# Performance work log

Hardware: AMD Instinct MI355X
Metric: run time of the kernel (lower is better)

## Reference

```python
import jax, jax.numpy as jnp
import numpy as np

N_NODES = 100000
N_EDGES = 800000
N_LABEL = 262144
IN, H, OUT = 16, 256, 128
BN_EPS = 1e-5


def setup_inputs() -> dict:
    key = jax.random.key(0)
    ks = jax.random.split(key, 32)
    def lin(k, fi, fo):
        return jax.random.normal(k, (fi, fo), jnp.float32) / np.sqrt(fi)
    inp = {
        "x": jax.random.normal(ks[0], (N_NODES, IN), jnp.float32),
        "edge_index": jax.random.randint(ks[1], (2, N_EDGES), 0, N_NODES, jnp.int32),
        "edge_weight": jax.random.uniform(ks[2], (N_EDGES,), jnp.float32),
        "edge_label_index": jax.random.randint(ks[3], (2, N_LABEL), 0, N_NODES, jnp.int32),
        # encoder GCN layers: 4 convs, BN on first 3
        "W1": lin(ks[4], IN, H),  "b1": jnp.zeros((H,), jnp.float32),
        "g1": jnp.ones((H,), jnp.float32), "be1": jnp.zeros((H,), jnp.float32),
        "W2": lin(ks[5], H, H),   "b2": jnp.zeros((H,), jnp.float32),
        "g2": jnp.ones((H,), jnp.float32), "be2": jnp.zeros((H,), jnp.float32),
        "W3": lin(ks[6], H, H),   "b3": jnp.zeros((H,), jnp.float32),
        "g3": jnp.ones((H,), jnp.float32), "be3": jnp.zeros((H,), jnp.float32),
        "W4": lin(ks[7], H, OUT), "b4": jnp.zeros((OUT,), jnp.float32),
        # decoder MLP on concatenated pair embeddings
        "D1W": lin(ks[8], 2 * OUT, OUT), "D1b": jnp.zeros((OUT,), jnp.float32),
        "D2W": lin(ks[9], OUT, OUT),     "D2b": jnp.zeros((OUT,), jnp.float32),
        "D3W": lin(ks[10], OUT, 1),      "D3b": jnp.zeros((1,), jnp.float32),
    }
    return inp


def _forward(x, edge_index, edge_weight, edge_label_index,
             W1, b1, g1, be1, W2, b2, g2, be2, W3, b3, g3, be3, W4, b4,
             D1W, D1b, D2W, D2b, D3W, D3b):
    n = x.shape[0]
    src, dst = edge_index[0], edge_index[1]
    # GCN symmetric normalization with self-loops (weight 1)
    deg = jax.ops.segment_sum(edge_weight, dst, num_segments=n) + 1.0
    dinv = jax.lax.rsqrt(deg)
    edge_norm = dinv[src] * edge_weight * dinv[dst]   # [E]
    self_norm = dinv * dinv                            # [N]

    def gcn(h, W, b):
        h = h @ W                                      # [N, F]
        agg = jax.ops.segment_sum(h[src] * edge_norm[:, None], dst, num_segments=n)
        return agg + h * self_norm[:, None] + b

    def bn(h, g, be):  # training-mode BatchNorm1d over node dim
        m = h.mean(axis=0)
        v = h.var(axis=0)
        return (h - m) * jax.lax.rsqrt(v + BN_EPS) * g + be

    h = jax.nn.relu(bn(gcn(x, W1, b1), g1, be1))
    h = jax.nn.relu(bn(gcn(h, W2, b2), g2, be2))
    h = jax.nn.relu(bn(gcn(h, W3, b3), g3, be3))
    z = gcn(h, W4, b4)                                 # [N, OUT] encoded

    # decode: gather both endpoints, concat, MLP + sigmoid
    e0, e1 = edge_label_index[0], edge_label_index[1]
    q = jnp.concatenate([z[e0], z[e1]], axis=1)        # [EL, 2*OUT]
    q = jax.nn.relu(q @ D1W + D1b)
    q = jax.nn.relu(q @ D2W + D2b)
    p = jax.nn.sigmoid(q @ D3W + D3b)
    return p.squeeze(-1)                               # [EL]


def reference(x, edge_index, edge_weight, edge_label_index,
              W1, b1, g1, be1, W2, b2, g2, be2, W3, b3, g3, be3, W4, b4,
              D1W, D1b, D2W, D2b, D3W, D3b):
    return _forward(x, edge_index, edge_weight, edge_label_index,
                    W1, b1, g1, be1, W2, b2, g2, be2, W3, b3, g3, be3, W4, b4,
                    D1W, D1b, D2W, D2b, D3W, D3b)
```

## Files before the change

kernel.cpp:

```cpp
#include <hip/hip_runtime.h>
#include <cmath>

#define NN 100000
#define NE 800000
#define NL 262144
#define GB 782
#define NP1 3125

typedef __attribute__((ext_vector_type(8))) short bf16x8;
typedef __attribute__((ext_vector_type(4))) float f32x4;

__device__ __forceinline__ unsigned short f2bf(float f) {
  unsigned int u = __builtin_bit_cast(unsigned int, f);
  u = (u + 0x7FFF + ((u >> 16) & 1)) >> 16;
  return (unsigned short)u;
}
__device__ __forceinline__ float bf2f(unsigned short u) {
  return __builtin_bit_cast(float, (unsigned int)u << 16);
}

__global__ void k_degcnt(const int* __restrict__ dst, const float* __restrict__ w,
                         unsigned long long* __restrict__ dc) {
  int e = blockIdx.x * 256 + threadIdx.x;
  if (e < NE) {
    unsigned long long pk = (1ULL << 32) | (unsigned long long)(unsigned int)(w[e] * 8388608.0f);
    atomicAdd(&dc[dst[e]], pk);
  }
}
__global__ void k_dinv2(const unsigned long long* __restrict__ dc,
                        float* __restrict__ dinv, int* __restrict__ cnt) {
  int n = blockIdx.x * 256 + threadIdx.x;
  if (n < NN) {
    unsigned long long v = dc[n];
    cnt[n] = (int)(v >> 32);
    dinv[n] = rsqrtf((float)(unsigned int)v * (1.0f / 8388608.0f) + 1.0f);
  }
}
__global__ void k_scan1(const int* __restrict__ cnt, int* __restrict__ tsum) {
  __shared__ int s[256];
  int t = threadIdx.x;
  int base = blockIdx.x * 1024;
  int acc = 0;
  for (int i = 0; i < 4; i++) { int idx = base + t * 4 + i; if (idx < NN) acc += cnt[idx]; }
  s[t] = acc; __syncthreads();
  for (int o = 128; o > 0; o >>= 1) { if (t < o) s[t] += s[t + o]; __syncthreads(); }
  if (t == 0) tsum[blockIdx.x] = s[0];
}
__global__ void k_scan2(const int* __restrict__ tsum, int* __restrict__ toff, int nt, int* __restrict__ rowptr_end) {
  __shared__ int s[256];
  int t = threadIdx.x;
  int v = (t < nt) ? tsum[t] : 0;
  s[t] = v; __syncthreads();
  for (int o = 1; o < 256; o <<= 1) { int xv = (t >= o) ? s[t - o] : 0; __syncthreads(); s[t] += xv; __syncthreads(); }
  if (t < nt) toff[t] = s[t] - v;
  if (t == 255) *rowptr_end = s[255];
}
__global__ void k_scan3(const int* __restrict__ cnt, const int* __restrict__ toff,
                        int* __restrict__ rowptr, int* __restrict__ nxt) {
  __shared__ int s[256];
  int t = threadIdx.x;
  int base = blockIdx.x * 1024 + t * 4;
  int v[4]; int tot = 0;
  for (int i = 0; i < 4; i++) { int idx = base + i; v[i] = (idx < NN) ? cnt[idx] : 0; tot += v[i]; }
  s[t] = tot; __syncthreads();
  for (int o = 1; o < 256; o <<= 1) { int xv = (t >= o) ? s[t - o] : 0; __syncthreads(); s[t] += xv; __syncthreads(); }
  int excl = s[t] - tot + toff[blockIdx.x];
  for (int i = 0; i < 4; i++) {
    int idx = base + i;
    if (idx < NN) { rowptr[idx] = excl; nxt[idx] = excl; }
    excl += v[i];
  }
}
__global__ void k_scatter2(const int* __restrict__ src, const int* __restrict__ dst, const float* __restrict__ w,
                           const float* __restrict__ dinv, int* __restrict__ nxt,
                           int* __restrict__ esp, float* __restrict__ enp) {
  int e = blockIdx.x * 256 + threadIdx.x;
  if (e < NE) {
    int d = dst[e], s = src[e];
    int p = atomicAdd(&nxt[d], 1);
    esp[p] = s; enp[p] = dinv[s] * w[e] * dinv[d];
  }
}

__global__ void k_cvt_wT(const float* __restrict__ W, unsigned short* __restrict__ Wt, int K, int N) {
  int id = blockIdx.x * 256 + threadIdx.x;
  if (id >= K * N) return;
  int n = id / K, k = id - n * K;
  Wt[id] = f2bf(W[k * N + n]);
}
__global__ void k_cvt_d1(const float* __restrict__ D1W, unsigned short* __restrict__ Wt) {
  int id = blockIdx.x * 256 + threadIdx.x;
  if (id >= 256 * 128) return;
  int n = id >> 7, k = id & 127;
  float v = (n < 128) ? D1W[(size_t)k * 128 + n] : D1W[(size_t)(128 + k) * 128 + (n - 128)];
  Wt[id] = f2bf(v);
}
__global__ void k_biasuv(const float* __restrict__ D1b, float* __restrict__ buv) {
  int t = threadIdx.x;
  buv[t] = (t < 128) ? D1b[t] : 0.f;
}

__global__ void k_pack(const unsigned short* __restrict__ Wt, unsigned short* __restrict__ P, int K, int NJ) {
  int id = blockIdx.x * 256 + threadIdx.x;
  int total = (K / 32) * NJ * 64;
  if (id >= total) return;
  int lane = id & 63, g = id >> 6;
  int j = g % NJ, s = g / NJ;
  int fr = lane & 15, fq = lane >> 4;
  uint4 v = *(const uint4*)(Wt + (size_t)(j * 16 + fr) * K + s * 32 + fq * 8);
  *(uint4*)(P + (size_t)id * 8) = v;
}

__global__ __launch_bounds__(256) void k_agg16(const float* __restrict__ x,
    const int* __restrict__ esp, const float* __restrict__ enp,
    const int* __restrict__ rowptr, const float* __restrict__ dinv,
    float* __restrict__ ax) {
  const int t = threadIdx.x;
  const int lane = t & 63;
  const int g = lane >> 2, gl = lane & 3;
  const int n = blockIdx.x * 64 + (t >> 6) * 16 + g;
  if (n >= NN) return;
  const float4* x4 = (const float4*)x;
  float d = dinv[n]; float dd = d * d;
  float4 self = x4[(size_t)n * 4 + gl];
  float4 acc = make_float4(self.x * dd, self.y * dd, self.z * dd, self.w * dd);
  const int i0 = rowptr[n];
  const int dg = rowptr[n + 1] - i0;
  int sreg[4]; float wreg[4];
  #pragma unroll
  for (int k = 0; k < 4; k++) {
    int idx = gl + 4 * k;
    if (idx < dg) { sreg[k] = esp[i0 + idx]; wreg[k] = enp[i0 + idx]; }
    else { sreg[k] = 0; wreg[k] = 0.f; }
  }
  const int gbase = lane & ~3;
  const int m4 = ((dg < 16 ? dg : 16) + 3) & ~3;
  #pragma unroll 4
  for (int e = 0; e < m4; e += 4) {
    int k = e >> 2;
    int s0, s1, s2, s3; float w0, w1, w2, w3;
    switch (k) {
      case 0: s0=__shfl(sreg[0],gbase|0); s1=__shfl(sreg[0],gbase|1); s2=__shfl(sreg[0],gbase|2); s3=__shfl(sreg[0],gbase|3);
              w0=__shfl(wreg[0],gbase|0); w1=__shfl(wreg[0],gbase|1); w2=__shfl(wreg[0],gbase|2); w3=__shfl(wreg[0],gbase|3); break;
      case 1: s0=__shfl(sreg[1],gbase|0); s1=__shfl(sreg[1],gbase|1); s2=__shfl(sreg[1],gbase|2); s3=__shfl(sreg[1],gbase|3);
              w0=__shfl(wreg[1],gbase|0); w1=__shfl(wreg[1],gbase|1); w2=__shfl(wreg[1],gbase|2); w3=__shfl(wreg[1],gbase|3); break;
      case 2: s0=__shfl(sreg[2],gbase|0); s1=__shfl(sreg[2],gbase|1); s2=__shfl(sreg[2],gbase|2); s3=__shfl(sreg[2],gbase|3);
              w0=__shfl(wreg[2],gbase|0); w1=__shfl(wreg[2],gbase|1); w2=__shfl(wreg[2],gbase|2); w3=__shfl(wreg[2],gbase|3); break;
      default: s0=__shfl(sreg[3],gbase|0); s1=__shfl(sreg[3],gbase|1); s2=__shfl(sreg[3],gbase|2); s3=__shfl(sreg[3],gbase|3);
              w0=__shfl(wreg[3],gbase|0); w1=__shfl(wreg[3],gbase|1); w2=__shfl(wreg[3],gbase|2); w3=__shfl(wreg[3],gbase|3); break;
    }
    float4 r0 = x4[(size_t)s0 * 4 + gl], r1 = x4[(size_t)s1 * 4 + gl];
    float4 r2 = x4[(size_t)s2 * 4 + gl], r3 = x4[(size_t)s3 * 4 + gl];
    acc.x += w0 * r0.x + w1 * r1.x + w2 * r2.x + w3 * r3.x;
    acc.y += w0 * r0.y + w1 * r1.y + w2 * r2.y + w3 * r3.y;
    acc.z += w0 * r0.z + w1 * r1.z + w2 * r2.z + w3 * r3.z;
    acc.w += w0 * r0.w + w1 * r1.w + w2 * r2.w + w3 * r3.w;
  }
  for (int i = i0 + 16; i < i0 + dg; i++) {
    int s0 = esp[i]; float w0 = enp[i];
    float4 r0 = x4[(size_t)s0 * 4 + gl];
    acc.x += w0 * r0.x; acc.y += w0 * r0.y; acc.z += w0 * r0.z; acc.w += w0 * r0.w;
  }
  ((float4*)ax)[(size_t)n * 4 + gl] = acc;
}

__global__ __launch_bounds__(256) void k_gemm16s(const float* __restrict__ ax, const float* __restrict__ W,
                                                 const float* __restrict__ b, unsigned short* __restrict__ out,
                                                 float* __restrict__ Ps, float* __restrict__ Pq) {
  __shared__ float xs[32][17];
  int t = threadIdx.x; int row0 = blockIdx.x * 32;
  for (int i = t; i < 512; i += 256) {
    int r = i >> 4, c = i & 15; int row = row0 + r;
    xs[r][c] = (row < NN) ? ax[(size_t)row * 16 + c] : 0.f;
  }
  float w[16];
  #pragma unroll
  for (int k = 0; k < 16; k++) w[k] = W[k * 256 + t];
  float bt = b[t];
  __syncthreads();
  float s_ = 0.f, q_ = 0.f;
  for (int r = 0; r < 32; r++) {
    int row = row0 + r; if (row >= NN) break;
    float acc = bt;
    #pragma unroll
    for (int k = 0; k < 16; k++) acc += xs[r][k] * w[k];
    out[(size_t)row * 256 + t] = f2bf(acc);
    s_ += acc; q_ += acc * acc;
  }
  Ps[(size_t)blockIdx.x * 256 + t] = s_;
  Pq[(size_t)blockIdx.x * 256 + t] = q_;
}

template <int KDIM, int NCOLS, bool STATS, bool BNA>
__global__ __launch_bounds__(512) void k_gemm_v12(
    const unsigned short* __restrict__ A, const unsigned short* __restrict__ Wp,
    const float* __restrict__ bias, const float* __restrict__ bnsc, const float* __restrict__ bnsh,
    unsigned short* __restrict__ C, float* __restrict__ Ps, float* __restrict__ Pq) {
  constexpr int CPW = NCOLS / 128;
  constexpr int KS = KDIM / 32;
  constexpr int LDA = KDIM + 8;
  constexpr int NU4 = KDIM / 32;
  __shared__ unsigned short S[128 * LDA];
  __shared__ float sc[BNA ? KDIM : 1], sh[BNA ? KDIM : 1];
  const int t = threadIdx.x;
  const int lane = t & 63, w = t >> 6, fr = lane & 15, fq = lane >> 4;
  const int row0 = blockIdx.x * 128;
  if (BNA) {
    if (t < KDIM) { sc[t] = bnsc[t]; sh[t] = bnsh[t]; }
    __syncthreads();
  }
  bf16x8 B[CPW][KS];
  #pragma unroll
  for (int c = 0; c < CPW; c++)
    #pragma unroll
    for (int s = 0; s < KS; s++)
      B[c][s] = *(const bf16x8*)(Wp + ((size_t)(s * (NCOLS / 16) + (w * CPW + c)) * 64 + lane) * 8);
  {
    int r = t >> 2, q = t & 3;
    int row = row0 + r;
    uint4* dst = (uint4*)(S + r * LDA + q * (KDIM / 4));
    if (row < NN) {
      const uint4* src = (const uint4*)(A + (size_t)row * KDIM + q * (KDIM / 4));
      #pragma unroll
      for (int i = 0; i < NU4; i++) {
        uint4 v = src[i];
        if (BNA) {
          unsigned int u[4] = {v.x, v.y, v.z, v.w};
          #pragma unroll
          for (int p = 0; p < 4; p++) {
            int colb = q * (KDIM / 4) + i * 8 + p * 2;
            float lo = fmaxf(bf2f((unsigned short)(u[p] & 0xFFFF)) * sc[colb] + sh[colb], 0.f);
            float hi = fmaxf(bf2f((unsigned short)(u[p] >> 16)) * sc[colb + 1] + sh[colb + 1], 0.f);
            u[p] = (unsigned int)f2bf(lo) | ((unsigned int)f2bf(hi) << 16);
          }
          v = make_uint4(u[0], u[1], u[2], u[3]);
        }
        dst[i] = v;
      }
    } else {
      #pragma unroll
      for (int i = 0; i < NU4; i++) dst[i] = make_uint4(0, 0, 0, 0);
    }
  }
  __syncthreads();
  f32x4 acc[8][CPW] = {};
  #pragma unroll
  for (int r = 0; r < 8; r++) {
    #pragma unroll
    for (int s = 0; s < KS; s++) {
      bf16x8 a = *(const bf16x8*)(S + (r * 16 + fr) * LDA + s * 32 + fq * 8);
      #pragma unroll
      for (int c = 0; c < CPW; c++)
        acc[r][c] = __builtin_amdgcn_mfma_f32_16x16x32_bf16(a, B[c][s], acc[r][c], 0, 0, 0);
    }
  }
  #pragma unroll
  for (int c = 0; c < CPW; c++) {
    const int col = w * (16 * CPW) + c * 16 + fr;
    float bj = bias[col];
    float s_ = 0.f, q_ = 0.f;
    #pragma unroll
    for (int r = 0; r < 8; r++) {
      #pragma unroll
      for (int rr = 0; rr < 4; rr++) {
        int row = row0 + r * 16 + fq * 4 + rr;
        if (row < NN) {
          float cv = acc[r][c][rr] + bj;
          C[(size_t)row * NCOLS + col] = f2bf(cv);
          if (STATS) { s_ += cv; q_ += cv * cv; }
        }
      }
    }
    if (STATS) {
      s_ += __shfl_xor(s_, 16); q_ += __shfl_xor(q_, 16);
      s_ += __shfl_xor(s_, 32); q_ += __shfl_xor(q_, 32);
      if (fq == 0) {
        Ps[(size_t)blockIdx.x * 256 + col] = s_;
        Pq[(size_t)blockIdx.x * 256 + col] = q_;
      }
    }
  }
}

__global__ __launch_bounds__(256) void k_bnred(const float* __restrict__ Ps, const float* __restrict__ Pq,
                                               const float* __restrict__ g, const float* __restrict__ be,
                                               float* __restrict__ scale, float* __restrict__ shift, int np) {
  __shared__ float Ss[256], Sq[256];
  const int f = blockIdx.x;
  const int t = threadIdx.x;
  float s = 0.f, q = 0.f;
  for (int p = t; p < np; p += 256) { s += Ps[(size_t)p * 256 + f]; q += Pq[(size_t)p * 256 + f]; }
  Ss[t] = s; Sq[t] = q;
  __syncthreads();
  for (int o = 128; o > 0; o >>= 1) { if (t < o) { Ss[t] += Ss[t + o]; Sq[t] += Sq[t + o]; } __syncthreads(); }
  if (t == 0) {
    float m = Ss[0] * (1.f / NN);
    float v = Sq[0] * (1.f / NN) - m * m;
    float sc = g[f] * rsqrtf(v + 1e-5f);
    scale[f] = sc; shift[f] = be[f] - m * sc;
  }
}

template <int FPL>
__device__ __forceinline__ void ldF(const unsigned short* p, float* f) {
  if constexpr (FPL == 8) {
    uint4 v = *(const uint4*)p;
    unsigned int u[4] = {v.x, v.y, v.z, v.w};
    #pragma unroll
    for (int i = 0; i < 4; i++) {
      f[2 * i] = bf2f((unsigned short)(u[i] & 0xFFFF));
      f[2 * i + 1] = bf2f((unsigned short)(u[i] >> 16));
    }
  } else {
    ushort4 v = *(const ushort4*)p;
    f[0] = bf2f(v.x); f[1] = bf2f(v.y); f[2] = bf2f(v.z); f[3] = bf2f(v.w);
  }
}
template <bool BN, int F>
__global__ __launch_bounds__(256) void k_agg5(const unsigned short* __restrict__ hb,
    const int* __restrict__ esp, const float* __restrict__ enp,
    const int* __restrict__ rowptr, const float* __restrict__ dinv,
    const float* __restrict__ scale, const float* __restrict__ shift,
    const float* __restrict__ bias, unsigned short* __restrict__ outb) {
  constexpr int FPL = F / 32;
  const int lane = threadIdx.x & 63;
  const int lg = lane & 31;
  const int srcbase = lane & 32;
  const int n = blockIdx.x * 8 + (threadIdx.x >> 5);
  const int f0 = lg * FPL;
  float sc8[FPL] = {}, sh8[FPL] = {};
  if constexpr (BN) {
    #pragma unroll
    for (int j = 0; j < FPL; j++) { sc8[j] = scale[f0 + j]; sh8[j] = shift[f0 + j]; }
  }
  auto xf = [&](float v, int j) -> float {
    if constexpr (BN) return fmaxf(v * sc8[j] + sh8[j], 0.f);
    else return v;
  };
  float d = dinv[n]; float dd = d * d;
  float acc[FPL];
  {
    float sv[FPL];
    ldF<FPL>(hb + (size_t)n * F + f0, sv);
    #pragma unroll
    for (int j = 0; j < FPL; j++) acc[j] = xf(sv[j], j) * dd + (BN ? 0.f : bias[f0 + j]);
  }
  const int i0 = rowptr[n];
  const int dg = rowptr[n + 1] - i0;
  int sreg = 0; float wreg = 0.f;
  if (lg < dg) { sreg = esp[i0 + lg]; wreg = enp[i0 + lg]; }
  const int m = (dg < 32) ? dg : 32;
  int e = 0;
  for (; e + 4 <= m; e += 4) {
    int s0 = __shfl(sreg, srcbase | e), s1 = __shfl(sreg, srcbase | (e + 1));
    int s2 = __shfl(sreg, srcbase | (e + 2)), s3 = __shfl(sreg, srcbase | (e + 3));
    float w0 = __shfl(wreg, srcbase | e), w1 = __shfl(wreg, srcbase | (e + 1));
    float w2 = __shfl(wreg, srcbase | (e + 2)), w3 = __shfl(wreg, srcbase | (e + 3));
    float r0[FPL], r1[FPL], r2[FPL], r3[FPL];
    ldF<FPL>(hb + (size_t)s0 * F + f0, r0);
    ldF<FPL>(hb + (size_t)s1 * F + f0, r1);
    ldF<FPL>(hb + (size_t)s2 * F + f0, r2);
    ldF<FPL>(hb + (size_t)s3 * F + f0, r3);
    #pragma unroll
    for (int j = 0; j < FPL; j++)
      acc[j] += w0 * xf(r0[j], j) + w1 * xf(r1[j], j) + w2 * xf(r2[j], j) + w3 * xf(r3[j], j);
  }
  for (; e < m; e++) {
    int s0 = __shfl(sreg, srcbase | e); float w0 = __shfl(wreg, srcbase | e);
    float r0[FPL];
    ldF<FPL>(hb + (size_t)s0 * F + f0, r0);
    #pragma unroll
    for (int j = 0; j < FPL; j++) acc[j] += w0 * xf(r0[j], j);
  }
  for (int i = i0 + 32; i < i0 + dg; i++) {
    int s0 = esp[i]; float w0 = enp[i];
    float r0[FPL];
    ldF<FPL>(hb + (size_t)s0 * F + f0, r0);
    #pragma unroll
    for (int j = 0; j < FPL; j++) acc[j] += w0 * xf(r0[j], j);
  }
  if constexpr (FPL == 8) {
    unsigned int o[4];
    #pragma unroll
    for (int i = 0; i < 4; i++)
      o[i] = (unsigned int)f2bf(acc[2 * i]) | ((unsigned int)f2bf(acc[2 * i + 1]) << 16);
    *(uint4*)(outb + (size_t)n * F + f0) = make_uint4(o[0], o[1], o[2], o[3]);
  } else {
    ushort4 o; o.x = f2bf(acc[0]); o.y = f2bf(acc[1]); o.z = f2bf(acc[2]); o.w = f2bf(acc[3]);
    *(ushort4*)(outb + (size_t)n * F + f0) = o;
  }
}

__global__ __launch_bounds__(256) void k_decoder3(
    const unsigned short* __restrict__ uv,
    const int* __restrict__ l0, const int* __restrict__ l1,
    const unsigned short* __restrict__ W2p, const float* __restrict__ D2b,
    const float* __restrict__ D3W, const float* __restrict__ D3b,
    float* __restrict__ out) {
  __shared__ unsigned short S[128 * 136];
  __shared__ int ei0[128], ei1[128];
  const int t = threadIdx.x;
  const int base = blockIdx.x * 128;
  if (t < 128) ei0[t] = l0[base + t];
  else ei1[t - 128] = l1[base + t - 128];
  __syncthreads();
  {
    int e = t >> 1, h = t & 1;
    const uint4* pu = (const uint4*)(uv + (size_t)ei0[e] * 256 + h * 64);
    const uint4* pv = (const uint4*)(uv + (size_t)ei1[e] * 256 + 128 + h * 64);
    uint4* dst = (uint4*)(S + e * 136 + h * 64);
    #pragma unroll
    for (int i = 0; i < 8; i++) {
      uint4 a = pu[i], b = pv[i];
      unsigned int ia[4] = {a.x, a.y, a.z, a.w};
      unsigned int ib[4] = {b.x, b.y, b.z, b.w};
      unsigned int o[4];
      #pragma unroll
      for (int p = 0; p < 4; p++) {
        float lo = fmaxf(bf2f((unsigned short)(ia[p] & 0xFFFF)) + bf2f((unsigned short)(ib[p] & 0xFFFF)), 0.f);
        float hi = fmaxf(bf2f((unsigned short)(ia[p] >> 16)) + bf2f((unsigned short)(ib[p] >> 16)), 0.f);
        o[p] = (unsigned int)f2bf(lo) | ((unsigned int)f2bf(hi) << 16);
      }
      dst[i] = make_uint4(o[0], o[1], o[2], o[3]);
    }
  }
  __syncthreads();
  const int lane = t & 63, w = t >> 6, fr = lane & 15, fq = lane >> 4;
  f32x4 acc2[2][8] = {};
  #pragma unroll
  for (int s = 0; s < 4; s++) {
    bf16x8 a0 = *(const bf16x8*)(S + (w * 32 + fr) * 136 + s * 32 + fq * 8);
    bf16x8 a1 = *(const bf16x8*)(S + (w * 32 + 16 + fr) * 136 + s * 32 + fq * 8);
    #pragma unroll
    for (int j = 0; j < 8; j++) {
      bf16x8 bw = *(const bf16x8*)(W2p + ((size_t)(s * 8 + j) * 64 + lane) * 8);
      acc2[0][j] = __builtin_amdgcn_mfma_f32_16x16x32_bf16(a0, bw, acc2[0][j], 0, 0, 0);
      acc2[1][j] = __builtin_amdgcn_mfma_f32_16x16x32_bf16(a1, bw, acc2[1][j], 0, 0, 0);
    }
  }
  float b2v[8], w3v[8];
  #pragma unroll
  for (int j = 0; j < 8; j++) { b2v[j] = D2b[j * 16 + fr]; w3v[j] = D3W[j * 16 + fr]; }
  float d3b = D3b[0];
  #pragma unroll
  for (int f = 0; f < 2; f++) {
    float p[4] = {0.f, 0.f, 0.f, 0.f};
    #pragma unroll
    for (int j = 0; j < 8; j++)
      #pragma unroll
      for (int r = 0; r < 4; r++)
        p[r] += fmaxf(acc2[f][j][r] + b2v[j], 0.f) * w3v[j];
    #pragma unroll
    for (int r = 0; r < 4; r++) {
      p[r] += __shfl_xor(p[r], 1);
      p[r] += __shfl_xor(p[r], 2);
      p[r] += __shfl_xor(p[r], 4);
      p[r] += __shfl_xor(p[r], 8);
      if (fr == 0) out[base + w * 32 + f * 16 + fq * 4 + r] = 1.f / (1.f + expf(-(p[r] + d3b)));
    }
  }
}

extern "C" void kernel_launch(void* const* d_in, const int* in_sizes, int n_in,
                              void* d_out, int out_size, void* d_ws, size_t ws_size,
                              hipStream_t stream) {
  const float* x = (const float*)d_in[0];
  const int* ei = (const int*)d_in[1];
  const int* esrc = ei; const int* edst = ei + NE;
  const float* ew = (const float*)d_in[2];
  const int* eli = (const int*)d_in[3];
  const int* l0 = eli; const int* l1 = eli + NL;
  const float* W1 = (const float*)d_in[4],  *b1 = (const float*)d_in[5];
  const float* g1 = (const float*)d_in[6],  *be1 = (const float*)d_in[7];
  const float* W2 = (const float*)d_in[8],  *b2 = (const float*)d_in[9];
  const float* g2 = (const float*)d_in[10], *be2 = (const float*)d_in[11];
  const float* W3 = (const float*)d_in[12], *b3 = (const float*)d_in[13];
  const float* g3 = (const float*)d_in[14], *be3 = (const float*)d_in[15];
  const float* W4 = (const float*)d_in[16], *b4 = (const float*)d_in[17];
  const float* D1W = (const float*)d_in[18], *D1b = (const float*)d_in[19];
  const float* D2W = (const float*)d_in[20], *D2b = (const float*)d_in[21];
  const float* D3W = (const float*)d_in[22], *D3b = (const float*)d_in[23];
  float* out = (float*)d_out;

  float* wf = (float*)d_ws;
  size_t off = 0;
  auto A = [&](size_t n) { float* p = wf + off; off += (n + 63) & ~(size_t)63; return p; };
  float* dinv = A(NN);
  float* enp = A(NE);
  float* scale = A(256);
  float* shift = A(256);
  float* buv = A(256);
  float* zero128 = A(128);
  float* Ps = A((size_t)NP1 * 256);
  float* Pq = A((size_t)NP1 * 256);
  float* axf = A((size_t)NN * 16);
  unsigned long long* dc = (unsigned long long*)A(2 * (size_t)NN);
  int* cnt = (int*)A(NN);
  int* rowptr = (int*)A(NN + 1);
  int* nxt = (int*)A(NN);
  int* esp = (int*)A(NE);
  int* tsum = (int*)A(256);
  int* toff = (int*)A(256);
  unsigned short* hbA = (unsigned short*)A((size_t)NN * 128);
  unsigned short* hbB = (unsigned short*)A((size_t)NN * 128);
  unsigned short* uv  = (unsigned short*)A((size_t)NN * 128);
  unsigned short* wt2 = (unsigned short*)A(256 * 128);
  unsigned short* wt3 = (unsigned short*)A(256 * 128);
  unsigned short* wt4 = (unsigned short*)A(128 * 128);
  unsigned short* wtD1 = (unsigned short*)A(128 * 128);
  unsigned short* w2t = (unsigned short*)A(64 * 128);
  unsigned short* wp2 = (unsigned short*)A(256 * 128);
  unsigned short* wp3 = (unsigned short*)A(256 * 128);
  unsigned short* wp4 = (unsigned short*)A(128 * 128);
  unsigned short* wpD1 = (unsigned short*)A(128 * 128);
  unsigned short* w2p = (unsigned short*)A(64 * 128);

  const int EB = (NE + 255) / 256;
  const int NB = (NN + 255) / 256;
  const int ST = (NN + 1023) / 1024;
  const int AB = NN / 8;
  const int AG16 = (NN + 63) / 64;

  hipMemsetAsync(dc, 0, (size_t)NN * 8, stream);
  hipMemsetAsync(zero128, 0, 128 * sizeof(float), stream);
  k_degcnt<<<EB, 256, 0, stream>>>(edst, ew, dc);
  k_dinv2<<<NB, 256, 0, stream>>>(dc, dinv, cnt);
  k_scan1<<<ST, 256, 0, stream>>>(cnt, tsum);
  k_scan2<<<1, 256, 0, stream>>>(tsum, toff, ST, rowptr + NN);
  k_scan3<<<ST, 256, 0, stream>>>(cnt, toff, rowptr, nxt);
  k_scatter2<<<EB, 256, 0, stream>>>(esrc, edst, ew, dinv, nxt, esp, enp);

  k_cvt_wT<<<(256 * 256 + 255) / 256, 256, 0, stream>>>(W2, wt2, 256, 256);
  k_cvt_wT<<<(256 * 256 + 255) / 256, 256, 0, stream>>>(W3, wt3, 256, 256);
  k_cvt_wT<<<(256 * 128 + 255) / 256, 256, 0, stream>>>(W4, wt4, 256, 128);
  k_cvt_d1<<<(256 * 128 + 255) / 256, 256, 0, stream>>>(D1W, wtD1);
  k_cvt_wT<<<(128 * 128 + 255) / 256, 256, 0, stream>>>(D2W, w2t, 128, 128);
  k_biasuv<<<1, 256, 0, stream>>>(D1b, buv);
  k_pack<<<32, 256, 0, stream>>>(wt2, wp2, 256, 16);
  k_pack<<<32, 256, 0, stream>>>(wt3, wp3, 256, 16);
  k_pack<<<16, 256, 0, stream>>>(wt4, wp4, 256, 8);
  k_pack<<<16, 256, 0, stream>>>(wtD1, wpD1, 128, 16);
  k_pack<<<8, 256, 0, stream>>>(w2t, w2p, 128, 8);

  k_agg16<<<AG16, 256, 0, stream>>>(x, esp, enp, rowptr, dinv, axf);
  k_gemm16s<<<NP1, 256, 0, stream>>>(axf, W1, b1, hbB, Ps, Pq);
  k_bnred<<<256, 256, 0, stream>>>(Ps, Pq, g1, be1, scale, shift, NP1);

  k_agg5<true, 256><<<AB, 256, 0, stream>>>(hbB, esp, enp, rowptr, dinv, scale, shift, nullptr, hbA);
  k_gemm_v12<256, 256, true, false><<<GB, 512, 0, stream>>>(hbA, wp2, b2, nullptr, nullptr, hbB, Ps, Pq);
  k_bnred<<<256, 256, 0, stream>>>(Ps, Pq, g2, be2, scale, shift, GB);

  k_agg5<true, 256><<<AB, 256, 0, stream>>>(hbB, esp, enp, rowptr, dinv, scale, shift, nullptr, hbA);
  k_gemm_v12<256, 256, true, false><<<GB, 512, 0, stream>>>(hbA, wp3, b3, nullptr, nullptr, hbB, Ps, Pq);
  k_bnred<<<256, 256, 0, stream>>>(Ps, Pq, g3, be3, scale, shift, GB);

  k_gemm_v12<256, 128, false, true><<<GB, 512, 0, stream>>>(hbB, wp4, zero128, scale, shift, hbA, nullptr, nullptr);
  k_agg5<false, 128><<<AB, 256, 0, stream>>>(hbA, esp, enp, rowptr, dinv, nullptr, nullptr, b4, hbB);
  k_gemm_v12<128, 256, false, false><<<GB, 512, 0, stream>>>(hbB, wpD1, buv, nullptr, nullptr, uv, nullptr, nullptr);

  k_decoder3<<<NL / 128, 256, 0, stream>>>(uv, l0, l1, w2p, D2b, D3W, D3b, out);
}
```

Baseline: 606.9 us.

## Fuse neighbor aggregation into the following MFMA GEMM via shared-memory tile

Adds a k_fused kernel that performs the GCN aggregation for 128 rows straight into a shared-memory bf16 tile, then runs the MFMA GEMM on that tile. It replaces the separate k_agg5 + k_gemm_v12 pairs for layers 2, 3 and the layer-4/decoder-D1 stage. The intent is to avoid writing and re-reading the aggregated intermediate through global memory and to cut kernel launches. In exchange, each 512-thread block handles 16 rows per pass over 8 serial passes, so there are fewer waves in flight to hide gather latency, and the weight registers plus the accumulator may limit occupancy.

New measurement: 686.8 us. 13.2% more time.

```diff
diff --git a/kernel.cpp b/kernel.cpp
--- a/kernel.cpp
+++ b/kernel.cpp
@@ -189,6 +189,164 @@
   }
   Ps[(size_t)blockIdx.x * 256 + t] = s_;
   Pq[(size_t)blockIdx.x * 256 + t] = q_;
+}
+
+template <int FPL>
+__device__ __forceinline__ void ldF(const unsigned short* p, float* f) {
+  if constexpr (FPL == 8) {
+    uint4 v = *(const uint4*)p;
+    unsigned int u[4] = {v.x, v.y, v.z, v.w};
+    #pragma unroll
+    for (int i = 0; i < 4; i++) {
+      f[2 * i] = bf2f((unsigned short)(u[i] & 0xFFFF));
+      f[2 * i + 1] = bf2f((unsigned short)(u[i] >> 16));
+    }
+  } else {
+    ushort4 v = *(const ushort4*)p;
+    f[0] = bf2f(v.x); f[1] = bf2f(v.y); f[2] = bf2f(v.z); f[3] = bf2f(v.w);
+  }
+}
+
+template <int KDIM, int NCOLS, bool STATS, bool BNG, bool BIASG>
+__global__ __launch_bounds__(512) void k_fused(
+    const unsigned short* __restrict__ src,
+    const int* __restrict__ esp, const float* __restrict__ enp,
+    const int* __restrict__ rowptr, const float* __restrict__ dinv,
+    const unsigned short* __restrict__ Wp,
+    const float* __restrict__ biasM, const float* __restrict__ bnsc, const float* __restrict__ bnsh,
+    const float* __restrict__ biasG,
+    unsigned short* __restrict__ C, float* __restrict__ Ps, float* __restrict__ Pq) {
+  constexpr int FPL = KDIM / 32;
+  constexpr int CPW = NCOLS / 128;
+  constexpr int KS = KDIM / 32;
+  constexpr int LDA = KDIM + 8;
+  __shared__ unsigned short S[128 * LDA];
+  const int t = threadIdx.x;
+  const int lane = t & 63, w = t >> 6, fr = lane & 15, fq = lane >> 4;
+  const int row0 = blockIdx.x * 128;
+  {
+    const int lg = lane & 31;
+    const int srcb = lane & 32;
+    const int hw = t >> 5;
+    const int f0 = lg * FPL;
+    float scR[FPL], shR[FPL], bgR[FPL];
+    if constexpr (BNG) {
+      #pragma unroll
+      for (int j = 0; j < FPL; j++) { scR[j] = bnsc[f0 + j]; shR[j] = bnsh[f0 + j]; }
+    }
+    if constexpr (BIASG) {
+      #pragma unroll
+      for (int j = 0; j < FPL; j++) bgR[j] = biasG[f0 + j];
+    }
+    auto xf = [&](float v, int j) -> float {
+      if constexpr (BNG) return fmaxf(v * scR[j] + shR[j], 0.f);
+      else return v;
+    };
+    for (int pass = 0; pass < 8; pass++) {
+      const int r = pass * 16 + hw;
+      const int n = row0 + r;
+      float acc[FPL];
+      #pragma unroll
+      for (int j = 0; j < FPL; j++) acc[j] = 0.f;
+      if (n < NN) {
+        float d = dinv[n]; float dd = d * d;
+        {
+          float sv[FPL];
+          ldF<FPL>(src + (size_t)n * KDIM + f0, sv);
+          #pragma unroll
+          for (int j = 0; j < FPL; j++) acc[j] = xf(sv[j], j) * dd + (BIASG ? bgR[j] : 0.f);
+        }
+        const int i0 = rowptr[n];
+        const int dg = rowptr[n + 1] - i0;
+        int sreg = 0; float wreg = 0.f;
+        if (lg < dg) { sreg = esp[i0 + lg]; wreg = enp[i0 + lg]; }
+        const int m = (dg < 32) ? dg : 32;
+        int e = 0;
+        for (; e + 4 <= m; e += 4) {
+          int s0 = __shfl(sreg, srcb | e), s1 = __shfl(sreg, srcb | (e + 1));
+          int s2 = __shfl(sreg, srcb | (e + 2)), s3 = __shfl(sreg, srcb | (e + 3));
+          float w0 = __shfl(wreg, srcb | e), w1 = __shfl(wreg, srcb | (e + 1));
+          float w2 = __shfl(wreg, srcb | (e + 2)), w3 = __shfl(wreg, srcb | (e + 3));
+          float r0[FPL], r1[FPL], r2[FPL], r3[FPL];
+          ldF<FPL>(src + (size_t)s0 * KDIM + f0, r0);
+          ldF<FPL>(src + (size_t)s1 * KDIM + f0, r1);
+          ldF<FPL>(src + (size_t)s2 * KDIM + f0, r2);
+          ldF<FPL>(src + (size_t)s3 * KDIM + f0, r3);
+          #pragma unroll
+          for (int j = 0; j < FPL; j++)
+            acc[j] += w0 * xf(r0[j], j) + w1 * xf(r1[j], j) + w2 * xf(r2[j], j) + w3 * xf(r3[j], j);
+        }
+        for (; e < m; e++) {
+          int s0 = __shfl(sreg, srcb | e); float w0 = __shfl(wreg, srcb | e);
+          float r0[FPL];
+          ldF<FPL>(src + (size_t)s0 * KDIM + f0, r0);
+          #pragma unroll
+          for (int j = 0; j < FPL; j++) acc[j] += w0 * xf(r0[j], j);
+        }
+        for (int i = i0 + 32; i < i0 + dg; i++) {
+          int s0 = esp[i]; float w0 = enp[i];
+          float r0[FPL];
+          ldF<FPL>(src + (size_t)s0 * KDIM + f0, r0);
+          #pragma unroll
+          for (int j = 0; j < FPL; j++) acc[j] += w0 * xf(r0[j], j);
+        }
+      }
+      if constexpr (FPL == 8) {
+        unsigned int o[4];
+        #pragma unroll
+        for (int i = 0; i < 4; i++)
+          o[i] = (unsigned int)f2bf(acc[2 * i]) | ((unsigned int)f2bf(acc[2 * i + 1]) << 16);
+        *(uint4*)(S + r * LDA + f0) = make_uint4(o[0], o[1], o[2], o[3]);
+      } else {
+        ushort4 o; o.x = f2bf(acc[0]); o.y = f2bf(acc[1]); o.z = f2bf(acc[2]); o.w = f2bf(acc[3]);
+        *(ushort4*)(S + r * LDA + f0) = o;
+      }
+    }
+  }
+  bf16x8 B[CPW][KS];
+  #pragma unroll
+  for (int c = 0; c < CPW; c++)
+    #pragma unroll
+    for (int s = 0; s < KS; s++)
+      B[c][s] = *(const bf16x8*)(Wp + ((size_t)(s * (NCOLS / 16) + (w * CPW + c)) * 64 + lane) * 8);
+  __syncthreads();
+  f32x4 acc[8][CPW] = {};
+  #pragma unroll
+  for (int r = 0; r < 8; r++) {
+    #pragma unroll
+    for (int s = 0; s < KS; s++) {
+      bf16x8 a = *(const bf16x8*)(S + (r * 16 + fr) * LDA + s * 32 + fq * 8);
+      #pragma unroll
+      for (int c = 0; c < CPW; c++)
+        acc[r][c] = __builtin_amdgcn_mfma_f32_16x16x32_bf16(a, B[c][s], acc[r][c], 0, 0, 0);
+    }
+  }
+  #pragma unroll
+  for (int c = 0; c < CPW; c++) {
+    const int col = w * (16 * CPW) + c * 16 + fr;
+    float bj = biasM[col];
+    float s_ = 0.f, q_ = 0.f;
+    #pragma unroll
+    for (int r = 0; r < 8; r++) {
+      #pragma unroll
+      for (int rr = 0; rr < 4; rr++) {
+        int row = row0 + r * 16 + fq * 4 + rr;
+        if (row < NN) {
+          float cv = acc[r][c][rr] + bj;
+          C[(size_t)row * NCOLS + col] = f2bf(cv);
+          if (STATS) { s_ += cv; q_ += cv * cv; }
+        }
+      }
+    }
+    if (STATS) {
+      s_ += __shfl_xor(s_, 16); q_ += __shfl_xor(q_, 16);
+      s_ += __shfl_xor(s_, 32); q_ += __shfl_xor(q_, 32);
+      if (fq == 0) {
+        Ps[(size_t)blockIdx.x * 256 + col] = s_;
+        Pq[(size_t)blockIdx.x * 256 + col] = q_;
+      }
+    }
+  }
 }
 
 template <int KDIM, int NCOLS, bool STATS, bool BNA>
@@ -298,96 +456,6 @@
     float v = Sq[0] * (1.f / NN) - m * m;
     float sc = g[f] * rsqrtf(v + 1e-5f);
     scale[f] = sc; shift[f] = be[f] - m * sc;
-  }
-}
-
-template <int FPL>
-__device__ __forceinline__ void ldF(const unsigned short* p, float* f) {
-  if constexpr (FPL == 8) {
-    uint4 v = *(const uint4*)p;
-    unsigned int u[4] = {v.x, v.y, v.z, v.w};
-    #pragma unroll
-    for (int i = 0; i < 4; i++) {
-      f[2 * i] = bf2f((unsigned short)(u[i] & 0xFFFF));
-      f[2 * i + 1] = bf2f((unsigned short)(u[i] >> 16));
-    }
-  } else {
-    ushort4 v = *(const ushort4*)p;
-    f[0] = bf2f(v.x); f[1] = bf2f(v.y); f[2] = bf2f(v.z); f[3] = bf2f(v.w);
-  }
-}
-template <bool BN, int F>
-__global__ __launch_bounds__(256) void k_agg5(const unsigned short* __restrict__ hb,
-    const int* __restrict__ esp, const float* __restrict__ enp,
-    const int* __restrict__ rowptr, const float* __restrict__ dinv,
-    const float* __restrict__ scale, const float* __restrict__ shift,
-    const float* __restrict__ bias, unsigned short* __restrict__ outb) {
-  constexpr int FPL = F / 32;
-  const int lane = threadIdx.x & 63;
-  const int lg = lane & 31;
-  const int srcbase = lane & 32;
-  const int n = blockIdx.x * 8 + (threadIdx.x >> 5);
-  const int f0 = lg * FPL;
-  float sc8[FPL] = {}, sh8[FPL] = {};
-  if constexpr (BN) {
-    #pragma unroll
-    for (int j = 0; j < FPL; j++) { sc8[j] = scale[f0 + j]; sh8[j] = shift[f0 + j]; }
-  }
-  auto xf = [&](float v, int j) -> float {
-    if constexpr (BN) return fmaxf(v * sc8[j] + sh8[j], 0.f);
-    else return v;
-  };
-  float d = dinv[n]; float dd = d * d;
-  float acc[FPL];
-  {
-    float sv[FPL];
-    ldF<FPL>(hb + (size_t)n * F + f0, sv);
-    #pragma unroll
-    for (int j = 0; j < FPL; j++) acc[j] = xf(sv[j], j) * dd + (BN ? 0.f : bias[f0 + j]);
-  }
-  const int i0 = rowptr[n];
-  const int dg = rowptr[n + 1] - i0;
-  int sreg = 0; float wreg = 0.f;
-  if (lg < dg) { sreg = esp[i0 + lg]; wreg = enp[i0 + lg]; }
-  const int m = (dg < 32) ? dg : 32;
-  int e = 0;
-  for (; e + 4 <= m; e += 4) {
-    int s0 = __shfl(sreg, srcbase | e), s1 = __shfl(sreg, srcbase | (e + 1));
-    int s2 = __shfl(sreg, srcbase | (e + 2)), s3 = __shfl(sreg, srcbase | (e + 3));
-    float w0 = __shfl(wreg, srcbase | e), w1 = __shfl(wreg, srcbase | (e + 1));
-    float w2 = __shfl(wreg, srcbase | (e + 2)), w3 = __shfl(wreg, srcbase | (e + 3));
-    float r0[FPL], r1[FPL], r2[FPL], r3[FPL];
-    ldF<FPL>(hb + (size_t)s0 * F + f0, r0);
-    ldF<FPL>(hb + (size_t)s1 * F + f0, r1);
-    ldF<FPL>(hb + (size_t)s2 * F + f0, r2);
-    ldF<FPL>(hb + (size_t)s3 * F + f0, r3);
-    #pragma unroll
-    for (int j = 0; j < FPL; j++)
-      acc[j] += w0 * xf(r0[j], j) + w1 * xf(r1[j], j) + w2 * xf(r2[j], j) + w3 * xf(r3[j], j);
-  }
-  for (; e < m; e++) {
-    int s0 = __shfl(sreg, srcbase | e); float w0 = __shfl(wreg, srcbase | e);
-    float r0[FPL];
-    ldF<FPL>(hb + (size_t)s0 * F + f0, r0);
-    #pragma unroll
-    for (int j = 0; j < FPL; j++) acc[j] += w0 * xf(r0[j], j);
-  }
-  for (int i = i0 + 32; i < i0 + dg; i++) {
-    int s0 = esp[i]; float w0 = enp[i];
-    float r0[FPL];
-    ldF<FPL>(hb + (size_t)s0 * F + f0, r0);
-    #pragma unroll
-    for (int j = 0; j < FPL; j++) acc[j] += w0 * xf(r0[j], j);
-  }
-  if constexpr (FPL == 8) {
-    unsigned int o[4];
-    #pragma unroll
-    for (int i = 0; i < 4; i++)
-      o[i] = (unsigned int)f2bf(acc[2 * i]) | ((unsigned int)f2bf(acc[2 * i + 1]) << 16);
-    *(uint4*)(outb + (size_t)n * F + f0) = make_uint4(o[0], o[1], o[2], o[3]);
-  } else {
-    ushort4 o; o.x = f2bf(acc[0]); o.y = f2bf(acc[1]); o.z = f2bf(acc[2]); o.w = f2bf(acc[3]);
-    *(ushort4*)(outb + (size_t)n * F + f0) = o;
   }
 }
 
@@ -518,7 +586,6 @@
   const int EB = (NE + 255) / 256;
   const int NB = (NN + 255) / 256;
   const int ST = (NN + 1023) / 1024;
-  const int AB = NN / 8;
   const int AG16 = (NN + 63) / 64;
 
   hipMemsetAsync(dc, 0, (size_t)NN * 8, stream);
@@ -546,17 +613,17 @@
   k_gemm16s<<<NP1, 256, 0, stream>>>(axf, W1, b1, hbB, Ps, Pq);
   k_bnred<<<256, 256, 0, stream>>>(Ps, Pq, g1, be1, scale, shift, NP1);
 
-  k_agg5<true, 256><<<AB, 256, 0, stream>>>(hbB, esp, enp, rowptr, dinv, scale, shift, nullptr, hbA);
-  k_gemm_v12<256, 256, true, false><<<GB, 512, 0, stream>>>(hbA, wp2, b2, nullptr, nullptr, hbB, Ps, Pq);
+  k_fused<256, 256, true, true, false><<<GB, 512, 0, stream>>>(
+      hbB, esp, enp, rowptr, dinv, wp2, b2, scale, shift, nullptr, hbA, Ps, Pq);
   k_bnred<<<256, 256, 0, stream>>>(Ps, Pq, g2, be2, scale, shift, GB);
 
-  k_agg5<true, 256><<<AB, 256, 0, stream>>>(hbB, esp, enp, rowptr, dinv, scale, shift, nullptr, hbA);
-  k_gemm_v12<256, 256, true, false><<<GB, 512, 0, stream>>>(hbA, wp3, b3, nullptr, nullptr, hbB, Ps, Pq);
+  k_fused<256, 256, true, true, false><<<GB, 512, 0, stream>>>(
+      hbA, esp, enp, rowptr, dinv, wp3, b3, scale, shift, nullptr, hbB, Ps, Pq);
   k_bnred<<<256, 256, 0, stream>>>(Ps, Pq, g3, be3, scale, shift, GB);
 
   k_gemm_v12<256, 128, false, true><<<GB, 512, 0, stream>>>(hbB, wp4, zero128, scale, shift, hbA, nullptr, nullptr);
-  k_agg5<false, 128><<<AB, 256, 0, stream>>>(hbA, esp, enp, rowptr, dinv, nullptr, nullptr, b4, hbB);
-  k_gemm_v12<128, 256, false, false><<<GB, 512, 0, stream>>>(hbB, wpD1, buv, nullptr, nullptr, uv, nullptr, nullptr);
+  k_fused<128, 256, false, false, true><<<GB, 512, 0, stream>>>(
+      hbA, esp, enp, rowptr, dinv, wpD1, buv, nullptr, nullptr, b4, uv, nullptr, nullptr);
 
   k_decoder3<<<NL / 128, 256, 0, stream>>>(uv, l0, l1, w2p, D2b, D3W, D3b, out);
 }
```
